# Optimization experiments

Measured on AMD Instinct MI355X. Metric: run time of the kernel, lower is better.

Reference implementation:

```python
import jax, jax.numpy as jnp
import numpy as np

N = 50000          # nodes
E = 1600000        # edges (avg degree 32)
D_IN = 128
D_OUT = 128
NEG_SLOPE = 0.01   # F.leaky_relu default (module ignores its negative_slope attr)


def setup_inputs() -> dict:
    key = jax.random.key(0)
    k = jax.random.split(key, 7)
    h = jax.random.normal(k[0], (N, D_IN), dtype=jnp.float32)
    embedding = jax.random.normal(k[1], (N, D_OUT), dtype=jnp.float32)
    # params (xavier-ish scaling)
    W_lin = jax.random.normal(k[2], (D_OUT, D_IN), dtype=jnp.float32) * (2.0 / (D_IN + D_OUT)) ** 0.5
    w_fc = jax.random.normal(k[3], (1, 2 * D_OUT), dtype=jnp.float32) * (2.0 / (2 * D_OUT + 1)) ** 0.5
    w_emb = jax.random.normal(k[4], (1, 2 * D_OUT), dtype=jnp.float32) * (2.0 / (2 * D_OUT + 1)) ** 0.5
    src = jax.random.randint(k[5], (E,), 0, N, dtype=jnp.int64 if jax.config.jax_enable_x64 else jnp.int32)
    dst = jax.random.randint(k[6], (E,), 0, N, dtype=jnp.int64 if jax.config.jax_enable_x64 else jnp.int32)
    return {"h": h, "embedding": embedding, "W_lin": W_lin, "w_fc": w_fc,
            "w_emb": w_emb, "src": src, "dst": dst}


def reference(h, embedding, W_lin, w_fc, w_emb, src, dst):
    n = h.shape[0]
    d = W_lin.shape[0]
    # z = lin(h): [N, out]
    z = h @ W_lin.T
    # attn_fc(cat(z_src, z_dst)) + attn_embed(cat(e_src, e_dst)) split into per-node
    # scalar scores so we gather [E] scalars instead of materializing [E, 2*out].
    s_fc_src = z @ w_fc[0, :d]            # [N]
    s_fc_dst = z @ w_fc[0, d:]            # [N]
    s_em_src = embedding @ w_emb[0, :d]   # [N]
    s_em_dst = embedding @ w_emb[0, d:]   # [N]
    a = (s_fc_src + s_em_src)[src] + (s_fc_dst + s_em_dst)[dst]   # [E]
    e = jnp.where(a > 0, a, NEG_SLOPE * a)  # leaky_relu, slope 0.01
    # segment softmax over incoming edges of each dst node
    m = jax.ops.segment_max(e, dst, num_segments=n)               # [N]
    e_exp = jnp.exp(e - m[dst])                                   # [E]
    denom = jax.ops.segment_sum(e_exp, dst, num_segments=n)       # [N]
    alpha = e_exp / denom[dst]                                    # [E]
    # weighted neighbor aggregation: h_out[v] = sum_{(u->v)} alpha * z[u]
    h_out = jax.ops.segment_sum(alpha[:, None] * z[src], dst, num_segments=n)
    return h_out
```

## Files before the change

### kernel.cpp

```cpp
#include <hip/hip_runtime.h>
#include <hip/hip_bf16.h>

#define D 128
#define BSH 7
#define BDST 128
#define NCHK 256
#define CAPB 5120
#define SL 8

typedef __attribute__((ext_vector_type(8))) short short8;
typedef __attribute__((ext_vector_type(4))) float f32x4;
typedef __attribute__((ext_vector_type(2))) float f32x2;

__device__ __forceinline__ unsigned short f2bf(float f) {
  unsigned u = __float_as_uint(f);
  unsigned r = (u + 0x7FFFu + ((u >> 16) & 1u)) >> 16;
  return (unsigned short)r;
}

__global__ __launch_bounds__(256) void k_wconv(const float* __restrict__ W,
                                               unsigned short* __restrict__ Wb) {
  const int i = blockIdx.x * 256 + threadIdx.x;
  float4 f = ((const float4*)W)[i];
  ushort4 o;
  o.x = f2bf(f.x); o.y = f2bf(f.y); o.z = f2bf(f.z); o.w = f2bf(f.w);
  ((ushort4*)Wb)[i] = o;
}

__global__ __launch_bounds__(256) void k_combo(
    const float* __restrict__ h, const unsigned short* __restrict__ Wb,
    const float* __restrict__ w_fc, const float* __restrict__ emb,
    const float* __restrict__ w_emb, unsigned* __restrict__ zd,
    float* __restrict__ a_src, float* __restrict__ a_dst,
    const int* __restrict__ src, const int* __restrict__ dst,
    int* __restrict__ bincur, unsigned* __restrict__ binrec,
    int n, int E, int NB, int CHSZ) {
  __shared__ int hl[512];
  __shared__ int cur[512];
  __shared__ float sfs[4][16], sfd[4][16];
  const int tid = threadIdx.x;

  if ((int)blockIdx.x < NCHK) {
    const int c = blockIdx.x;
    for (int i = tid; i < NB; i += 256) hl[i] = 0;
    __syncthreads();
    const int beg = c * CHSZ, end = min(beg + CHSZ, E);
    for (int i = beg + tid; i < end; i += 256) atomicAdd(&hl[dst[i] >> BSH], 1);
    __syncthreads();
    for (int b = tid; b < NB; b += 256) {
      int cb = hl[b];
      cur[b] = cb > 0 ? atomicAdd(&bincur[b], cb) : 0;
    }
    __syncthreads();
    for (int i = beg + tid; i < end; i += 256) {
      int d = dst[i];
      int b = d >> BSH;
      int pos = atomicAdd(&cur[b], 1);
      binrec[(size_t)b * CAPB + pos] =
          ((unsigned)src[i] << BSH) | (unsigned)(d & (BDST - 1));
    }
    return;
  }

  const int lane = tid & 63;
  const int wid = tid >> 6;
  const int m0 = (blockIdx.x - NCHK) * 64 + wid * 16;
  if (m0 >= n) return;
  const int c = lane & 15;
  const int g = lane >> 4;

  int arow = m0 + c;
  if (arow >= n) arow = n - 1;
  const float4* hrow = (const float4*)(h + (size_t)arow * 128);

  short8 afr[4];
#pragma unroll
  for (int s = 0; s < 4; ++s) {
    float4 f0 = hrow[8 * s + 2 * g];
    float4 f1 = hrow[8 * s + 2 * g + 1];
    short8 a;
    a[0] = (short)f2bf(f0.x); a[1] = (short)f2bf(f0.y);
    a[2] = (short)f2bf(f0.z); a[3] = (short)f2bf(f0.w);
    a[4] = (short)f2bf(f1.x); a[5] = (short)f2bf(f1.y);
    a[6] = (short)f2bf(f1.z); a[7] = (short)f2bf(f1.w);
    afr[s] = a;
  }

  f32x4 acc[8];
#pragma unroll
  for (int t = 0; t < 8; ++t) acc[t] = (f32x4){0.f, 0.f, 0.f, 0.f};

#pragma unroll
  for (int s = 0; s < 4; ++s) {
#pragma unroll
    for (int t = 0; t < 8; ++t) {
      short8 b = *(const short8*)(Wb + ((size_t)(t * 16 + c) * 128 + 32 * s + 8 * g));
      acc[t] = __builtin_amdgcn_mfma_f32_16x16x32_bf16(afr[s], b, acc[t], 0, 0, 0);
    }
  }

  float wfs[8], wfd[8];
#pragma unroll
  for (int t = 0; t < 8; ++t) {
    wfs[t] = w_fc[t * 16 + c];
    wfd[t] = w_fc[128 + t * 16 + c];
  }

  const int rbase = m0 + 4 * g;
#pragma unroll
  for (int r = 0; r < 4; ++r) {
    const int row = rbase + r;
    if (row < n) {
#pragma unroll
      for (int tp = 0; tp < 4; ++tp) {
        unsigned dw = ((unsigned)f2bf(acc[tp + 4][r]) << 16) | (unsigned)f2bf(acc[tp][r]);
        zd[(size_t)row * 64 + tp * 16 + c] = dw;
      }
    }
    float ps = 0.f, pd = 0.f;
#pragma unroll
    for (int t = 0; t < 8; ++t) {
      ps += acc[t][r] * wfs[t];
      pd += acc[t][r] * wfd[t];
    }
#pragma unroll
    for (int off = 1; off < 16; off <<= 1) {
      ps += __shfl_xor(ps, off, 64);
      pd += __shfl_xor(pd, off, 64);
    }
    if (c == 0) {
      sfs[wid][4 * g + r] = ps;
      sfd[wid][4 * g + r] = pd;
    }
  }
  __syncthreads();

  const int nloc = lane >> 2;
  const int qc = lane & 3;
  const int node2 = m0 + nloc;
  float es = 0.f, ed = 0.f;
  if (node2 < n) {
    const float4* er = (const float4*)(emb + (size_t)node2 * 128 + qc * 32);
    const float4* wsp = (const float4*)(w_emb + qc * 32);
    const float4* wdp = (const float4*)(w_emb + 128 + qc * 32);
#pragma unroll
    for (int j = 0; j < 8; ++j) {
      float4 e4 = er[j], s4 = wsp[j], d4 = wdp[j];
      es += e4.x * s4.x + e4.y * s4.y + e4.z * s4.z + e4.w * s4.w;
      ed += e4.x * d4.x + e4.y * d4.y + e4.z * d4.z + e4.w * d4.w;
    }
  }
  es += __shfl_xor(es, 1, 64); es += __shfl_xor(es, 2, 64);
  ed += __shfl_xor(ed, 1, 64); ed += __shfl_xor(ed, 2, 64);
  if (qc == 0 && node2 < n) {
    a_src[node2] = es + sfs[wid][nloc];
    a_dst[node2] = ed + sfd[wid][nloc];
  }
}

__global__ __launch_bounds__(256) void k_build(const unsigned* __restrict__ binrec,
                                               const int* __restrict__ bincur,
                                               int2* __restrict__ row2,
                                               int* __restrict__ csr, int n) {
  __shared__ int hist[BDST * SL];
  __shared__ int excl[BDST * SL];
  __shared__ int sh[256];
  const int tid = threadIdx.x, b = blockIdx.x;
  const int cntb = bincur[b];
  const unsigned* rb = binrec + (size_t)b * CAPB;
  const int base = b * CAPB;

  for (int k = tid; k < BDST * SL; k += 256) hist[k] = 0;
  __syncthreads();
  for (int i = tid; i < cntb; i += 256) {
    unsigned r = rb[i];
    int dl = r & (BDST - 1);
    int sv = (int)(r >> BSH);
    atomicAdd(&hist[dl * SL + (sv >> 13)], 1);
  }
  __syncthreads();
  const int k0 = tid * 4;
  int v4[4], s = 0;
#pragma unroll
  for (int j = 0; j < 4; ++j) { v4[j] = hist[k0 + j]; s += v4[j]; }
  sh[tid] = s;
  __syncthreads();
  for (int off = 1; off < 256; off <<= 1) {
    int a = (tid >= off) ? sh[tid - off] : 0;
    __syncthreads();
    sh[tid] += a;
    __syncthreads();
  }
  int e0 = sh[tid] - s;
#pragma unroll
  for (int j = 0; j < 4; ++j) { excl[k0 + j] = e0; e0 += v4[j]; }
  __syncthreads();
  if (tid < BDST) {
    int bg = excl[tid * SL];
    int en = (tid == BDST - 1) ? cntb : excl[(tid + 1) * SL];
    int v = b * BDST + tid;
    if (v < n) row2[v] = make_int2(base + bg, base + en);
  }
  __syncthreads();
  for (int i = tid; i < cntb; i += 256) {
    unsigned r = rb[i];
    int dl = r & (BDST - 1);
    int sv = (int)(r >> BSH);
    int pos = base + atomicAdd(&excl[dl * SL + (sv >> 13)], 1);
    csr[pos] = sv;
  }
}

__global__ __launch_bounds__(256) void k_agg(const unsigned* __restrict__ zd,
                                             const float* __restrict__ a_src,
                                             const float* __restrict__ a_dst,
                                             const int2* __restrict__ row2,
                                             const int* __restrict__ csr,
                                             float* __restrict__ out, int n) {
  const int lane = threadIdx.x & 63;
  const int grp = lane >> 4;
  const int sub = lane & 15;
  const int v = blockIdx.x * 4 + (threadIdx.x >> 6);
  if (v >= n) return;
  const int2 be = row2[v];
  const int beg = be.x, end = be.y;
  const float adv = a_dst[v];

  f32x2 acc2[4];
#pragma unroll
  for (int j = 0; j < 4; ++j) acc2[j] = (f32x2){0.f, 0.f};
  float ews = 0.f;

#pragma unroll 4
  for (int i = beg + grp; i < end; i += 4) {
    const int u = csr[i];
    const float a = a_src[u] + adv;
    const float e = a > 0.f ? a : 0.01f * a;
    const float ew = __expf(e);
    const uint4 zz = ((const uint4*)zd)[(size_t)u * 16 + sub];
    ews += ew;
    const f32x2 ew2 = {ew, ew};
    f32x2 z0 = {__uint_as_float(zz.x << 16), __uint_as_float(zz.x & 0xffff0000u)};
    f32x2 z1 = {__uint_as_float(zz.y << 16), __uint_as_float(zz.y & 0xffff0000u)};
    f32x2 z2 = {__uint_as_float(zz.z << 16), __uint_as_float(zz.z & 0xffff0000u)};
    f32x2 z3 = {__uint_as_float(zz.w << 16), __uint_as_float(zz.w & 0xffff0000u)};
    acc2[0] += ew2 * z0;
    acc2[1] += ew2 * z1;
    acc2[2] += ew2 * z2;
    acc2[3] += ew2 * z3;
  }

#pragma unroll
  for (int off = 16; off <= 32; off <<= 1) {
    ews += __shfl_xor(ews, off, 64);
#pragma unroll
    for (int j = 0; j < 4; ++j) {
      acc2[j][0] += __shfl_xor(acc2[j][0], off, 64);
      acc2[j][1] += __shfl_xor(acc2[j][1], off, 64);
    }
  }

  if (grp == 0) {
    const float inv = (end > beg) ? 1.f / ews : 0.f;
    float4 olo = make_float4(acc2[0][0] * inv, acc2[1][0] * inv, acc2[2][0] * inv, acc2[3][0] * inv);
    float4 ohi = make_float4(acc2[0][1] * inv, acc2[1][1] * inv, acc2[2][1] * inv, acc2[3][1] * inv);
    ((float4*)out)[(size_t)v * 32 + sub] = olo;
    ((float4*)out)[(size_t)v * 32 + 16 + sub] = ohi;
  }
}

extern "C" void kernel_launch(void* const* d_in, const int* in_sizes, int n_in,
                              void* d_out, int out_size, void* d_ws, size_t ws_size,
                              hipStream_t stream) {
  const float* h = (const float*)d_in[0];
  const float* emb = (const float*)d_in[1];
  const float* W = (const float*)d_in[2];
  const float* wfc = (const float*)d_in[3];
  const float* wemb = (const float*)d_in[4];
  const int* src = (const int*)d_in[5];
  const int* dst = (const int*)d_in[6];
  const int n = in_sizes[0] / D;
  const int E = in_sizes[5];
  const int NB = (n + BDST - 1) >> BSH;
  const int CHSZ = (E + NCHK - 1) / NCHK;
  const int NLIN = (n + 63) / 64;

  char* ws = (char*)d_ws;
  size_t off = 0;
  auto alloc = [&](size_t bytes) {
    void* p = ws + off;
    off = (off + bytes + 255) & ~(size_t)255;
    return p;
  };
  unsigned* zd = (unsigned*)alloc((size_t)n * 64 * 4);
  unsigned short* Wb = (unsigned short*)alloc(D * D * 2);
  float* a_src = (float*)alloc((size_t)n * 4);
  float* a_dst = (float*)alloc((size_t)n * 4);
  int* bincur = (int*)alloc((size_t)NB * 4);
  int2* row2 = (int2*)alloc((size_t)n * 8);
  unsigned* binrec = (unsigned*)alloc((size_t)NB * CAPB * 4);
  int* csr = (int*)alloc((size_t)NB * CAPB * 4);
  (void)off;
  (void)ws_size;

  (void)hipMemsetAsync(bincur, 0, (size_t)NB * 4, stream);
  k_wconv<<<(D * D / 4 + 255) / 256, 256, 0, stream>>>(W, Wb);
  k_combo<<<NCHK + NLIN, 256, 0, stream>>>(h, Wb, wfc, emb, wemb, zd, a_src, a_dst,
                                           src, dst, bincur, binrec, n, E, NB, CHSZ);
  k_build<<<NB, 256, 0, stream>>>(binrec, bincur, row2, csr, n);
  k_agg<<<(n + 3) / 4, 256, 0, stream>>>(zd, a_src, a_dst, row2, csr, (float*)d_out, n);
}
```

Baseline: 124.7 us.

## Stage binned edge records in shared memory for coalesced scatter to global bins

The binning phase of k_combo now places each chunk's edge records into a shared-memory buffer sorted by destination bin, using a local prefix sum over per-bin counts. It then writes them to the global bin arrays in a second pass, so consecutive threads write contiguous runs instead of scattering single records. The chunk count doubles so each chunk fits the shared buffer. The record encoding changes to pack the full dst in the low 16 bits and src in the high bits, and k_build is updated to match. The cost is a larger shared-memory footprint in a kernel that also runs the GEMM path, which may lower occupancy. The new packing also assumes node ids fit in 16 bits, which does not hold for N=50000 sources in 16 bits shifted... src<<16 limits src below 65536.

```diff
diff --git a/kernel.cpp b/kernel.cpp
--- a/kernel.cpp
+++ b/kernel.cpp
@@ -4,7 +4,8 @@
 #define D 128
 #define BSH 7
 #define BDST 128
-#define NCHK 256
+#define NCHK 512
+#define CHCAP 3200
 #define CAPB 5120
 #define SL 8
 
@@ -35,29 +36,50 @@
     const int* __restrict__ src, const int* __restrict__ dst,
     int* __restrict__ bincur, unsigned* __restrict__ binrec,
     int n, int E, int NB, int CHSZ) {
-  __shared__ int hl[512];
-  __shared__ int cur[512];
+  __shared__ unsigned recbuf[CHCAP];
+  __shared__ int hl[512], gbase[512], loff[512], lcur[512];
+  __shared__ int sh[256];
   __shared__ float sfs[4][16], sfd[4][16];
   const int tid = threadIdx.x;
 
   if ((int)blockIdx.x < NCHK) {
     const int c = blockIdx.x;
-    for (int i = tid; i < NB; i += 256) hl[i] = 0;
-    __syncthreads();
     const int beg = c * CHSZ, end = min(beg + CHSZ, E);
+    const int cnt = end - beg;
+    for (int i = tid; i < 512; i += 256) { hl[i] = 0; lcur[i] = 0; }
+    __syncthreads();
     for (int i = beg + tid; i < end; i += 256) atomicAdd(&hl[dst[i] >> BSH], 1);
     __syncthreads();
     for (int b = tid; b < NB; b += 256) {
       int cb = hl[b];
-      cur[b] = cb > 0 ? atomicAdd(&bincur[b], cb) : 0;
-    }
+      gbase[b] = cb > 0 ? atomicAdd(&bincur[b], cb) : 0;
+    }
+    int v0 = hl[2 * tid], v1 = hl[2 * tid + 1];
+    int s = v0 + v1;
+    sh[tid] = s;
+    __syncthreads();
+    for (int off = 1; off < 256; off <<= 1) {
+      int a = (tid >= off) ? sh[tid - off] : 0;
+      __syncthreads();
+      sh[tid] += a;
+      __syncthreads();
+    }
+    int base = sh[tid] - s;
+    loff[2 * tid] = base;
+    loff[2 * tid + 1] = base + v0;
     __syncthreads();
     for (int i = beg + tid; i < end; i += 256) {
       int d = dst[i];
       int b = d >> BSH;
-      int pos = atomicAdd(&cur[b], 1);
-      binrec[(size_t)b * CAPB + pos] =
-          ((unsigned)src[i] << BSH) | (unsigned)(d & (BDST - 1));
+      unsigned r = ((unsigned)src[i] << 16) | (unsigned)d;
+      int lp = atomicAdd(&lcur[b], 1);
+      recbuf[loff[b] + lp] = r;
+    }
+    __syncthreads();
+    for (int i = tid; i < cnt; i += 256) {
+      unsigned r = recbuf[i];
+      int b = (int)(r & 0xFFFFu) >> BSH;
+      binrec[(size_t)b * CAPB + gbase[b] + (i - loff[b])] = r;
     }
     return;
   }
@@ -175,7 +197,7 @@
   for (int i = tid; i < cntb; i += 256) {
     unsigned r = rb[i];
     int dl = r & (BDST - 1);
-    int sv = (int)(r >> BSH);
+    int sv = (int)(r >> 16);
     atomicAdd(&hist[dl * SL + (sv >> 13)], 1);
   }
   __syncthreads();
@@ -205,7 +227,7 @@
   for (int i = tid; i < cntb; i += 256) {
     unsigned r = rb[i];
     int dl = r & (BDST - 1);
-    int sv = (int)(r >> BSH);
+    int sv = (int)(r >> 16);
     int pos = base + atomicAdd(&excl[dl * SL + (sv >> 13)], 1);
     csr[pos] = sv;
   }
```

Result: no change. 126.5 us (+1.5%).

## Precompute edge weights in CSR build and fold bincur zeroing into wconv

Applied to the files above, without the earlier changes.

Moves the per-edge leaky-relu and exp computation from the aggregation kernel into the CSR build kernel, storing (src, weight) pairs so k_agg no longer does a dependent gather of a_src per edge. The memset of bincur is removed and the zeroing is folded into the weight-conversion kernel launch. This saves a launch and shortens the dependent-load chain in the hot loop, at the cost of doubling the CSR array size and adding random a_src gathers to k_build.

```diff
diff --git a/kernel.cpp b/kernel.cpp
--- a/kernel.cpp
+++ b/kernel.cpp
@@ -19,8 +19,10 @@
 }
 
 __global__ __launch_bounds__(256) void k_wconv(const float* __restrict__ W,
-                                               unsigned short* __restrict__ Wb) {
+                                               unsigned short* __restrict__ Wb,
+                                               int* __restrict__ bincur, int NB) {
   const int i = blockIdx.x * 256 + threadIdx.x;
+  if (i < NB) bincur[i] = 0;
   float4 f = ((const float4*)W)[i];
   ushort4 o;
   o.x = f2bf(f.x); o.y = f2bf(f.y); o.z = f2bf(f.z); o.w = f2bf(f.w);
@@ -42,7 +44,7 @@
 
   if ((int)blockIdx.x < NCHK) {
     const int c = blockIdx.x;
-    for (int i = tid; i < NB; i += 256) hl[i] = 0;
+    for (int i = tid; i < 512; i += 256) hl[i] = 0;
     __syncthreads();
     const int beg = c * CHSZ, end = min(beg + CHSZ, E);
     for (int i = beg + tid; i < end; i += 256) atomicAdd(&hl[dst[i] >> BSH], 1);
@@ -160,17 +162,24 @@
 
 __global__ __launch_bounds__(256) void k_build(const unsigned* __restrict__ binrec,
                                                const int* __restrict__ bincur,
+                                               const float* __restrict__ a_src,
+                                               const float* __restrict__ a_dst,
                                                int2* __restrict__ row2,
-                                               int* __restrict__ csr, int n) {
+                                               int2* __restrict__ csr2, int n) {
   __shared__ int hist[BDST * SL];
   __shared__ int excl[BDST * SL];
   __shared__ int sh[256];
+  __shared__ float adl[BDST];
   const int tid = threadIdx.x, b = blockIdx.x;
   const int cntb = bincur[b];
   const unsigned* rb = binrec + (size_t)b * CAPB;
   const int base = b * CAPB;
 
   for (int k = tid; k < BDST * SL; k += 256) hist[k] = 0;
+  if (tid < BDST) {
+    int v = b * BDST + tid;
+    adl[tid] = (v < n) ? a_dst[v] : 0.f;
+  }
   __syncthreads();
   for (int i = tid; i < cntb; i += 256) {
     unsigned r = rb[i];
@@ -206,16 +215,17 @@
     unsigned r = rb[i];
     int dl = r & (BDST - 1);
     int sv = (int)(r >> BSH);
+    float a = a_src[sv] + adl[dl];
+    float e = a > 0.f ? a : 0.01f * a;
+    float ew = __expf(e);
     int pos = base + atomicAdd(&excl[dl * SL + (sv >> 13)], 1);
-    csr[pos] = sv;
+    csr2[pos] = make_int2(sv, __float_as_int(ew));
   }
 }
 
 __global__ __launch_bounds__(256) void k_agg(const unsigned* __restrict__ zd,
-                                             const float* __restrict__ a_src,
-                                             const float* __restrict__ a_dst,
                                              const int2* __restrict__ row2,
-                                             const int* __restrict__ csr,
+                                             const int2* __restrict__ csr2,
                                              float* __restrict__ out, int n) {
   const int lane = threadIdx.x & 63;
   const int grp = lane >> 4;
@@ -224,7 +234,6 @@
   if (v >= n) return;
   const int2 be = row2[v];
   const int beg = be.x, end = be.y;
-  const float adv = a_dst[v];
 
   f32x2 acc2[4];
 #pragma unroll
@@ -233,11 +242,9 @@
 
 #pragma unroll 4
   for (int i = beg + grp; i < end; i += 4) {
-    const int u = csr[i];
-    const float a = a_src[u] + adv;
-    const float e = a > 0.f ? a : 0.01f * a;
-    const float ew = __expf(e);
-    const uint4 zz = ((const uint4*)zd)[(size_t)u * 16 + sub];
+    const int2 e2 = csr2[i];
+    const float ew = __int_as_float(e2.y);
+    const uint4 zz = ((const uint4*)zd)[(size_t)e2.x * 16 + sub];
     ews += ew;
     const f32x2 ew2 = {ew, ew};
     f32x2 z0 = {__uint_as_float(zz.x << 16), __uint_as_float(zz.x & 0xffff0000u)};
@@ -299,14 +306,13 @@
   int* bincur = (int*)alloc((size_t)NB * 4);
   int2* row2 = (int2*)alloc((size_t)n * 8);
   unsigned* binrec = (unsigned*)alloc((size_t)NB * CAPB * 4);
-  int* csr = (int*)alloc((size_t)NB * CAPB * 4);
+  int2* csr2 = (int2*)alloc((size_t)NB * CAPB * 8);
   (void)off;
   (void)ws_size;
 
-  (void)hipMemsetAsync(bincur, 0, (size_t)NB * 4, stream);
-  k_wconv<<<(D * D / 4 + 255) / 256, 256, 0, stream>>>(W, Wb);
+  k_wconv<<<(D * D / 4 + 255) / 256, 256, 0, stream>>>(W, Wb, bincur, NB);
   k_combo<<<NCHK + NLIN, 256, 0, stream>>>(h, Wb, wfc, emb, wemb, zd, a_src, a_dst,
                                            src, dst, bincur, binrec, n, E, NB, CHSZ);
-  k_build<<<NB, 256, 0, stream>>>(binrec, bincur, row2, csr, n);
-  k_agg<<<(n + 3) / 4, 256, 0, stream>>>(zd, a_src, a_dst, row2, csr, (float*)d_out, n);
-}
+  k_build<<<NB, 256, 0, stream>>>(binrec, bincur, a_src, a_dst, row2, csr2, n);
+  k_agg<<<(n + 3) / 4, 256, 0, stream>>>(zd, row2, csr2, (float*)d_out, n);
+}
```

Measured after the change: 126.4 us. About the same (+1.4%).
